# Kernel tuning notes

Measured on AMD Instinct MI355X. Metric: run time of the kernel, lower is better.

## Reference

```python
import jax, jax.numpy as jnp
import numpy as np

NUM_ITERATIONS = 3


def squash(t, axis=-1):
    # scale * t / sqrt(||t||^2 + eps), scale = ||t||^2 / (1 + ||t||^2)
    sq = jnp.sum(t * t, axis=axis, keepdims=True)
    return (sq / (1.0 + sq)) * t / jnp.sqrt(sq + 1e-8)


def setup_inputs() -> dict:
    key = jax.random.key(0)
    k1, k2 = jax.random.split(key)
    B, C, R, I, O = 128, 10, 8192, 8, 16
    x = jax.random.normal(k1, (B, R, I), dtype=jnp.float32)
    route_weights = jax.random.normal(k2, (C, R, I, O), dtype=jnp.float32) * 0.1
    return {"x": x, "route_weights": route_weights}


def reference(x, route_weights):
    # x: [B, R, I]; route_weights: [C, R, I, O]
    u_hat = jnp.einsum('bri,crio->bcro', x, route_weights)  # [B, C, R, O]
    B, C, R, O = u_hat.shape
    b_ij = jnp.zeros((B, C, R), dtype=u_hat.dtype)
    v_j = None
    for it in range(NUM_ITERATIONS):
        c_ij = jax.nn.softmax(b_ij, axis=1)                 # [B, C, R]
        s_j = jnp.einsum('bcr,bcro->bco', c_ij, u_hat)      # [B, C, O]
        v_j = squash(s_j, axis=-1)                          # [B, C, O]
        if it < NUM_ITERATIONS - 1:
            a_ij = jnp.einsum('bcro,bco->bcr', u_hat, v_j)  # [B, C, R]
            b_ij = b_ij + a_ij
    return v_j
```

## Files before the change

kernel.cpp:

```cpp
#include <hip/hip_runtime.h>
#include <hip/hip_fp16.h>
#include <math.h>

#define B_ 128
#define C_ 10
#define R_ 8192
#define I_ 8
#define O_ 16

typedef __attribute__((ext_vector_type(8))) _Float16 half8;
typedef __attribute__((ext_vector_type(16))) float f32x16;

#define XROW 512
#define WROW 64
#define WZERO 80
#define SBO (C_ * B_ * O_)

__device__ __forceinline__ unsigned pk2(float a, float b) {
    __half2 h = __floats2half2_rn(a, b);
    return *(unsigned*)&h;
}

__global__ __launch_bounds__(256, 4) void fused_iter(const float* __restrict__ x,
                                                     const float* __restrict__ w,
                                                     const float* __restrict__ vsum,
                                                     __half* __restrict__ part,
                                                     int mode) {
    __shared__ unsigned xls[8 * XROW];
    __shared__ unsigned wls[(80 + 1) * WROW];

    const int tid = threadIdx.x;
    const int wave = tid >> 6;
    const int lane = tid & 63;
    const int n = lane & 31;
    const int g = lane >> 5;
    const int rp_m = (lane & 31) >> 4;
    const int o_m = lane & 15;
    const int b = wave * 32 + n;
    const int r0 = blockIdx.x * 8;

#pragma unroll
    for (int k = 0; k < 8; ++k) {
        const int f = k * 256 + tid;
        const int bb = f >> 4;
        const int rr = (f >> 1) & 7;
        const int q = f & 1;
        const float4 v = *(const float4*)(x + ((size_t)bb * R_ + r0 + rr) * 8 + q * 4);
        *(uint2*)(xls + rr * XROW + bb * 4 + q * 2) = make_uint2(pk2(v.x, v.y), pk2(v.z, v.w));
    }
#pragma unroll
    for (int k = 0; k < 5; ++k) {
        const int id = k * 256 + tid;
        const int o = id & 15;
        const int r = (id >> 4) & 7;
        const int c = id >> 7;
        const float* wp = w + ((size_t)(c * R_ + r0 + r) * 8) * 16 + o;
        const float f0 = wp[0],  f1 = wp[16],  f2 = wp[32],  f3 = wp[48];
        const float f4 = wp[64], f5 = wp[80],  f6 = wp[96],  f7 = wp[112];
        *(uint4*)(wls + (c * 8 + r) * WROW + o * 4) =
            make_uint4(pk2(f0, f1), pk2(f2, f3), pk2(f4, f5), pk2(f6, f7));
    }
    if (tid < WROW) wls[WZERO * WROW + tid] = 0u;
    __syncthreads();

    const int act = (g == rp_m);

    half8 xbr[4];
#pragma unroll
    for (int rp = 0; rp < 4; ++rp)
        xbr[rp] = *(const half8*)(xls + (2 * rp + g) * XROW + b * 4);

    f32x16 zero16;
#pragma unroll
    for (int j = 0; j < 16; ++j) zero16[j] = 0.f;

    if (mode) {
        float dinv[4];
        {
            float dacc[4] = {0.f, 0.f, 0.f, 0.f};
#pragma unroll 1
            for (int c = 0; c < C_; ++c) {
                const float4* vp = (const float4*)(vsum + ((size_t)c * B_ + b) * O_ + 4 * g);
                const float4 va = vp[0];
                const float4 vb = vp[2];
#pragma unroll
                for (int rp = 0; rp < 4; ++rp) {
                    const int woff = act ? ((c * 8 + 2 * rp + g) * WROW + o_m * 4)
                                         : (WZERO * WROW);
                    const half8 a = *(const half8*)(wls + woff);
                    const f32x16 u = __builtin_amdgcn_mfma_f32_32x32x16_f16(a, xbr[rp], zero16, 0, 0, 0);
                    const float p0 = u[0] * va.x + u[1] * va.y + u[2] * va.z + u[3] * va.w
                                   + u[4] * vb.x + u[5] * vb.y + u[6] * vb.z + u[7] * vb.w;
                    const float p1 = u[8] * va.x + u[9] * va.y + u[10] * va.z + u[11] * va.w
                                   + u[12] * vb.x + u[13] * vb.y + u[14] * vb.z + u[15] * vb.w;
                    const float send = g ? p0 : p1;
                    const float recv = __shfl_xor(send, 32);
                    const float pg = (g ? p1 : p0) + recv;
                    dacc[rp] += __expf(pg);
                }
            }
#pragma unroll
            for (int rp = 0; rp < 4; ++rp) dinv[rp] = 1.0f / dacc[rp];
        }

#pragma unroll 1
        for (int c = 0; c < C_; ++c) {
            const float4* vp = (const float4*)(vsum + ((size_t)c * B_ + b) * O_ + 4 * g);
            const float4 va = vp[0];
            const float4 vb = vp[2];
            f32x16 acc;
#pragma unroll
            for (int rp = 0; rp < 4; ++rp) {
                const int woff = act ? ((c * 8 + 2 * rp + g) * WROW + o_m * 4)
                                     : (WZERO * WROW);
                const half8 a = *(const half8*)(wls + woff);
                const f32x16 u = __builtin_amdgcn_mfma_f32_32x32x16_f16(a, xbr[rp], zero16, 0, 0, 0);
                const float p0 = u[0] * va.x + u[1] * va.y + u[2] * va.z + u[3] * va.w
                               + u[4] * vb.x + u[5] * vb.y + u[6] * vb.z + u[7] * vb.w;
                const float p1 = u[8] * va.x + u[9] * va.y + u[10] * va.z + u[11] * va.w
                               + u[12] * vb.x + u[13] * vb.y + u[14] * vb.z + u[15] * vb.w;
                const float send = g ? p0 : p1;
                const float recv = __shfl_xor(send, 32);
                const float pg = (g ? p1 : p0) + recv;
                const float w_own = __expf(pg) * dinv[rp];
                const float w_oth = __shfl_xor(w_own, 32);
                const float c0 = g ? w_oth : w_own;
                const float c1 = g ? w_own : w_oth;
                if (rp == 0) {
#pragma unroll
                    for (int j = 0; j < 8; ++j)  acc[j] = c0 * u[j];
#pragma unroll
                    for (int j = 8; j < 16; ++j) acc[j] = c1 * u[j];
                } else {
#pragma unroll
                    for (int j = 0; j < 8; ++j)  acc[j] += c0 * u[j];
#pragma unroll
                    for (int j = 8; j < 16; ++j) acc[j] += c1 * u[j];
                }
            }
            const float f0 = acc[0] + acc[8],  f1 = acc[1] + acc[9];
            const float f2 = acc[2] + acc[10], f3 = acc[3] + acc[11];
            const float f4 = acc[4] + acc[12], f5 = acc[5] + acc[13];
            const float f6 = acc[6] + acc[14], f7 = acc[7] + acc[15];
            __half* pp = part + (((size_t)blockIdx.x * C_ + c) * B_ + b) * O_;
            *(uint2*)(pp + 4 * g)     = make_uint2(pk2(f0, f1), pk2(f2, f3));
            *(uint2*)(pp + 8 + 4 * g) = make_uint2(pk2(f4, f5), pk2(f6, f7));
        }
    } else {
#pragma unroll 1
        for (int c = 0; c < C_; ++c) {
            f32x16 acc = zero16;
#pragma unroll
            for (int rp = 0; rp < 4; ++rp) {
                const int woff = act ? ((c * 8 + 2 * rp + g) * WROW + o_m * 4)
                                     : (WZERO * WROW);
                const half8 a = *(const half8*)(wls + woff);
                acc = __builtin_amdgcn_mfma_f32_32x32x16_f16(a, xbr[rp], acc, 0, 0, 0);
            }
            const float f0 = (acc[0] + acc[8])  * 0.1f, f1 = (acc[1] + acc[9])  * 0.1f;
            const float f2 = (acc[2] + acc[10]) * 0.1f, f3 = (acc[3] + acc[11]) * 0.1f;
            const float f4 = (acc[4] + acc[12]) * 0.1f, f5 = (acc[5] + acc[13]) * 0.1f;
            const float f6 = (acc[6] + acc[14]) * 0.1f, f7 = (acc[7] + acc[15]) * 0.1f;
            __half* pp = part + (((size_t)blockIdx.x * C_ + c) * B_ + b) * O_;
            *(uint2*)(pp + 4 * g)     = make_uint2(pk2(f0, f1), pk2(f2, f3));
            *(uint2*)(pp + 8 + 4 * g) = make_uint2(pk2(f4, f5), pk2(f6, f7));
        }
    }
}

__global__ __launch_bounds__(256) void reduce1(const __half* __restrict__ part,
                                               float* __restrict__ part2) {
    const int t8 = blockIdx.x * 256 + threadIdx.x;
    const __half* p = part + (size_t)(blockIdx.y * 64) * SBO + (size_t)t8 * 8;
    float s0 = 0.f, s1 = 0.f, s2 = 0.f, s3 = 0.f;
    float s4 = 0.f, s5 = 0.f, s6 = 0.f, s7 = 0.f;
#pragma unroll 8
    for (int s = 0; s < 64; ++s) {
        const uint4 v = *(const uint4*)(p + (size_t)s * SBO);
        const __half2 h0 = *(const __half2*)&v.x;
        const __half2 h1 = *(const __half2*)&v.y;
        const __half2 h2 = *(const __half2*)&v.z;
        const __half2 h3 = *(const __half2*)&v.w;
        const float2 f0 = __half22float2(h0);
        const float2 f1 = __half22float2(h1);
        const float2 f2 = __half22float2(h2);
        const float2 f3 = __half22float2(h3);
        s0 += f0.x; s1 += f0.y; s2 += f1.x; s3 += f1.y;
        s4 += f2.x; s5 += f2.y; s6 += f3.x; s7 += f3.y;
    }
    float* q = part2 + (size_t)blockIdx.y * SBO + (size_t)t8 * 8;
    *(float4*)q       = make_float4(s0, s1, s2, s3);
    *(float4*)(q + 4) = make_float4(s4, s5, s6, s7);
}

__global__ __launch_bounds__(256) void finish_pass(const float* __restrict__ part2,
                                                   float* __restrict__ vsum,
                                                   float* __restrict__ out,
                                                   int mode) {
    const int t = blockIdx.x * 256 + threadIdx.x;
    float sum = 0.f;
#pragma unroll
    for (int s = 0; s < 16; ++s)
        sum += part2[(size_t)s * SBO + t];

    float sq = sum * sum;
    sq += __shfl_xor(sq, 1);
    sq += __shfl_xor(sq, 2);
    sq += __shfl_xor(sq, 4);
    sq += __shfl_xor(sq, 8);
    const float scale = sq / ((1.0f + sq) * sqrtf(sq + 1e-8f));
    const float v = scale * sum;

    if (mode == 0) {
        vsum[t] = v;
    } else if (mode == 1) {
        vsum[t] += v;
    } else {
        const int o = t & 15, b = (t >> 4) & 127, c = t >> 11;
        out[((size_t)b * C_ + c) * O_ + o] = v;
    }
}

extern "C" void kernel_launch(void* const* d_in, const int* in_sizes, int n_in,
                              void* d_out, int out_size, void* d_ws, size_t ws_size,
                              hipStream_t stream) {
    const float* x = (const float*)d_in[0];
    const float* w = (const float*)d_in[1];
    float* out = (float*)d_out;

    __half* part = (__half*)d_ws;
    float* part2 = (float*)(part + (size_t)1024 * SBO);
    float* vsum  = part2 + (size_t)16 * SBO;

    const dim3 fgrid(R_ / 8);
    const dim3 rgrid(10, 16);
    const dim3 ggrid(80);

    fused_iter<<<fgrid, 256, 0, stream>>>(x, w, vsum, part, 0);
    reduce1<<<rgrid, 256, 0, stream>>>(part, part2);
    finish_pass<<<ggrid, 256, 0, stream>>>(part2, vsum, out, 0);

    fused_iter<<<fgrid, 256, 0, stream>>>(x, w, vsum, part, 1);
    reduce1<<<rgrid, 256, 0, stream>>>(part, part2);
    finish_pass<<<ggrid, 256, 0, stream>>>(part2, vsum, out, 1);

    fused_iter<<<fgrid, 256, 0, stream>>>(x, w, vsum, part, 1);
    reduce1<<<rgrid, 256, 0, stream>>>(part, part2);
    finish_pass<<<ggrid, 256, 0, stream>>>(part2, vsum, out, 2);
}
```

Measured before the change: 218.6 us.

## Process two capsule classes per iteration, swizzle x LDS layout, widen reduction grid

The per-class loops now handle two classes per iteration, issuing two independent MFMAs so their latencies can overlap, and the weighted accumulation is folded directly into 8 accumulators. The x tile in LDS gets an XOR swizzle on the column index to reduce bank conflicts when each wave reads its B operand. The first-stage reduction uses 32 slices instead of 64 per block, giving twice as many blocks for better parallelism, while the finish pass now sums 32 partials instead of 16. Register pressure rises from holding two MFMA results at once, which may hurt occupancy under the 4-blocks launch bound.

Result: slower. 350.3 us (+60.3%).

```diff
diff --git a/kernel.cpp b/kernel.cpp
--- a/kernel.cpp
+++ b/kernel.cpp
@@ -15,10 +15,20 @@
 #define WROW 64
 #define WZERO 80
 #define SBO (C_ * B_ * O_)
+#define NRED 32
 
 __device__ __forceinline__ unsigned pk2(float a, float b) {
     __half2 h = __floats2half2_rn(a, b);
     return *(unsigned*)&h;
+}
+
+__device__ __forceinline__ float dot8lo(const f32x16& u, const float4& va, const float4& vb) {
+    return u[0] * va.x + u[1] * va.y + u[2] * va.z + u[3] * va.w
+         + u[4] * vb.x + u[5] * vb.y + u[6] * vb.z + u[7] * vb.w;
+}
+__device__ __forceinline__ float dot8hi(const f32x16& u, const float4& va, const float4& vb) {
+    return u[8] * va.x + u[9] * va.y + u[10] * va.z + u[11] * va.w
+         + u[12] * vb.x + u[13] * vb.y + u[14] * vb.z + u[15] * vb.w;
 }
 
 __global__ __launch_bounds__(256, 4) void fused_iter(const float* __restrict__ x,
@@ -46,7 +56,8 @@
         const int rr = (f >> 1) & 7;
         const int q = f & 1;
         const float4 v = *(const float4*)(x + ((size_t)bb * R_ + r0 + rr) * 8 + q * 4);
-        *(uint2*)(xls + rr * XROW + bb * 4 + q * 2) = make_uint2(pk2(v.x, v.y), pk2(v.z, v.w));
+        *(uint2*)(xls + rr * XROW + (((bb * 4 + q * 2) ^ (rr << 2)))) =
+            make_uint2(pk2(v.x, v.y), pk2(v.z, v.w));
     }
 #pragma unroll
     for (int k = 0; k < 5; ++k) {
@@ -67,8 +78,10 @@
 
     half8 xbr[4];
 #pragma unroll
-    for (int rp = 0; rp < 4; ++rp)
-        xbr[rp] = *(const half8*)(xls + (2 * rp + g) * XROW + b * 4);
+    for (int rp = 0; rp < 4; ++rp) {
+        const int row = 2 * rp + g;
+        xbr[rp] = *(const half8*)(xls + row * XROW + ((b * 4) ^ (row << 2)));
+    }
 
     f32x16 zero16;
 #pragma unroll
@@ -79,24 +92,28 @@
         {
             float dacc[4] = {0.f, 0.f, 0.f, 0.f};
 #pragma unroll 1
-            for (int c = 0; c < C_; ++c) {
-                const float4* vp = (const float4*)(vsum + ((size_t)c * B_ + b) * O_ + 4 * g);
-                const float4 va = vp[0];
-                const float4 vb = vp[2];
+            for (int c = 0; c < C_; c += 2) {
+                const float4* vpA = (const float4*)(vsum + ((size_t)c * B_ + b) * O_ + 4 * g);
+                const float4* vpB = (const float4*)(vsum + ((size_t)(c + 1) * B_ + b) * O_ + 4 * g);
+                const float4 vaA = vpA[0], vbA = vpA[2];
+                const float4 vaB = vpB[0], vbB = vpB[2];
 #pragma unroll
                 for (int rp = 0; rp < 4; ++rp) {
-                    const int woff = act ? ((c * 8 + 2 * rp + g) * WROW + o_m * 4)
-                                         : (WZERO * WROW);
-                    const half8 a = *(const half8*)(wls + woff);
-                    const f32x16 u = __builtin_amdgcn_mfma_f32_32x32x16_f16(a, xbr[rp], zero16, 0, 0, 0);
-                    const float p0 = u[0] * va.x + u[1] * va.y + u[2] * va.z + u[3] * va.w
-                                   + u[4] * vb.x + u[5] * vb.y + u[6] * vb.z + u[7] * vb.w;
-                    const float p1 = u[8] * va.x + u[9] * va.y + u[10] * va.z + u[11] * va.w
-                                   + u[12] * vb.x + u[13] * vb.y + u[14] * vb.z + u[15] * vb.w;
-                    const float send = g ? p0 : p1;
-                    const float recv = __shfl_xor(send, 32);
-                    const float pg = (g ? p1 : p0) + recv;
-                    dacc[rp] += __expf(pg);
+                    const int woffA = act ? ((c * 8 + 2 * rp + g) * WROW + o_m * 4)
+                                          : (WZERO * WROW);
+                    const int woffB = act ? (((c + 1) * 8 + 2 * rp + g) * WROW + o_m * 4)
+                                          : (WZERO * WROW);
+                    const half8 aA = *(const half8*)(wls + woffA);
+                    const half8 aB = *(const half8*)(wls + woffB);
+                    const f32x16 uA = __builtin_amdgcn_mfma_f32_32x32x16_f16(aA, xbr[rp], zero16, 0, 0, 0);
+                    const f32x16 uB = __builtin_amdgcn_mfma_f32_32x32x16_f16(aB, xbr[rp], zero16, 0, 0, 0);
+                    const float pA0 = dot8lo(uA, vaA, vbA), pA1 = dot8hi(uA, vaA, vbA);
+                    const float pB0 = dot8lo(uB, vaB, vbB), pB1 = dot8hi(uB, vaB, vbB);
+                    const float recvA = __shfl_xor(g ? pA0 : pA1, 32);
+                    const float recvB = __shfl_xor(g ? pB0 : pB1, 32);
+                    const float pgA = (g ? pA1 : pA0) + recvA;
+                    const float pgB = (g ? pB1 : pB0) + recvB;
+                    dacc[rp] += __expf(pgA) + __expf(pgB);
                 }
             }
 #pragma unroll
@@ -104,66 +121,74 @@
         }
 
 #pragma unroll 1
-        for (int c = 0; c < C_; ++c) {
-            const float4* vp = (const float4*)(vsum + ((size_t)c * B_ + b) * O_ + 4 * g);
-            const float4 va = vp[0];
-            const float4 vb = vp[2];
-            f32x16 acc;
+        for (int c = 0; c < C_; c += 2) {
+            const float4* vpA = (const float4*)(vsum + ((size_t)c * B_ + b) * O_ + 4 * g);
+            const float4* vpB = (const float4*)(vsum + ((size_t)(c + 1) * B_ + b) * O_ + 4 * g);
+            const float4 vaA = vpA[0], vbA = vpA[2];
+            const float4 vaB = vpB[0], vbB = vpB[2];
+            float accA[8], accB[8];
+#pragma unroll
+            for (int j = 0; j < 8; ++j) { accA[j] = 0.f; accB[j] = 0.f; }
 #pragma unroll
             for (int rp = 0; rp < 4; ++rp) {
-                const int woff = act ? ((c * 8 + 2 * rp + g) * WROW + o_m * 4)
-                                     : (WZERO * WROW);
-                const half8 a = *(const half8*)(wls + woff);
-                const f32x16 u = __builtin_amdgcn_mfma_f32_32x32x16_f16(a, xbr[rp], zero16, 0, 0, 0);
-                const float p0 = u[0] * va.x + u[1] * va.y + u[2] * va.z + u[3] * va.w
-                               + u[4] * vb.x + u[5] * vb.y + u[6] * vb.z + u[7] * vb.w;
-                const float p1 = u[8] * va.x + u[9] * va.y + u[10] * va.z + u[11] * va.w
-                               + u[12] * vb.x + u[13] * vb.y + u[14] * vb.z + u[15] * vb.w;
-                const float send = g ? p0 : p1;
-                const float recv = __shfl_xor(send, 32);
-                const float pg = (g ? p1 : p0) + recv;
-                const float w_own = __expf(pg) * dinv[rp];
-                const float w_oth = __shfl_xor(w_own, 32);
-                const float c0 = g ? w_oth : w_own;
-                const float c1 = g ? w_own : w_oth;
-                if (rp == 0) {
-#pragma unroll
-                    for (int j = 0; j < 8; ++j)  acc[j] = c0 * u[j];
-#pragma unroll
-                    for (int j = 8; j < 16; ++j) acc[j] = c1 * u[j];
-                } else {
-#pragma unroll
-                    for (int j = 0; j < 8; ++j)  acc[j] += c0 * u[j];
-#pragma unroll
-                    for (int j = 8; j < 16; ++j) acc[j] += c1 * u[j];
+                const int woffA = act ? ((c * 8 + 2 * rp + g) * WROW + o_m * 4)
+                                      : (WZERO * WROW);
+                const int woffB = act ? (((c + 1) * 8 + 2 * rp + g) * WROW + o_m * 4)
+                                      : (WZERO * WROW);
+                const half8 aA = *(const half8*)(wls + woffA);
+                const half8 aB = *(const half8*)(wls + woffB);
+                const f32x16 uA = __builtin_amdgcn_mfma_f32_32x32x16_f16(aA, xbr[rp], zero16, 0, 0, 0);
+                const f32x16 uB = __builtin_amdgcn_mfma_f32_32x32x16_f16(aB, xbr[rp], zero16, 0, 0, 0);
+                const float pA0 = dot8lo(uA, vaA, vbA), pA1 = dot8hi(uA, vaA, vbA);
+                const float pB0 = dot8lo(uB, vaB, vbB), pB1 = dot8hi(uB, vaB, vbB);
+                const float recvA = __shfl_xor(g ? pA0 : pA1, 32);
+                const float recvB = __shfl_xor(g ? pB0 : pB1, 32);
+                const float pgA = (g ? pA1 : pA0) + recvA;
+                const float pgB = (g ? pB1 : pB0) + recvB;
+                const float wA = __expf(pgA) * dinv[rp];
+                const float wB = __expf(pgB) * dinv[rp];
+                const float wAo = __shfl_xor(wA, 32);
+                const float wBo = __shfl_xor(wB, 32);
+                const float cA0 = g ? wAo : wA, cA1 = g ? wA : wAo;
+                const float cB0 = g ? wBo : wB, cB1 = g ? wB : wBo;
+#pragma unroll
+                for (int j = 0; j < 8; ++j) {
+                    accA[j] += cA0 * uA[j] + cA1 * uA[j + 8];
+                    accB[j] += cB0 * uB[j] + cB1 * uB[j + 8];
                 }
             }
-            const float f0 = acc[0] + acc[8],  f1 = acc[1] + acc[9];
-            const float f2 = acc[2] + acc[10], f3 = acc[3] + acc[11];
-            const float f4 = acc[4] + acc[12], f5 = acc[5] + acc[13];
-            const float f6 = acc[6] + acc[14], f7 = acc[7] + acc[15];
-            __half* pp = part + (((size_t)blockIdx.x * C_ + c) * B_ + b) * O_;
-            *(uint2*)(pp + 4 * g)     = make_uint2(pk2(f0, f1), pk2(f2, f3));
-            *(uint2*)(pp + 8 + 4 * g) = make_uint2(pk2(f4, f5), pk2(f6, f7));
+            __half* ppA = part + (((size_t)blockIdx.x * C_ + c) * B_ + b) * O_;
+            *(uint2*)(ppA + 4 * g)     = make_uint2(pk2(accA[0], accA[1]), pk2(accA[2], accA[3]));
+            *(uint2*)(ppA + 8 + 4 * g) = make_uint2(pk2(accA[4], accA[5]), pk2(accA[6], accA[7]));
+            __half* ppB = part + (((size_t)blockIdx.x * C_ + (c + 1)) * B_ + b) * O_;
+            *(uint2*)(ppB + 4 * g)     = make_uint2(pk2(accB[0], accB[1]), pk2(accB[2], accB[3]));
+            *(uint2*)(ppB + 8 + 4 * g) = make_uint2(pk2(accB[4], accB[5]), pk2(accB[6], accB[7]));
         }
     } else {
 #pragma unroll 1
-        for (int c = 0; c < C_; ++c) {
-            f32x16 acc = zero16;
+        for (int c = 0; c < C_; c += 2) {
+            f32x16 accA = zero16, accB = zero16;
 #pragma unroll
             for (int rp = 0; rp < 4; ++rp) {
-                const int woff = act ? ((c * 8 + 2 * rp + g) * WROW + o_m * 4)
-                                     : (WZERO * WROW);
-                const half8 a = *(const half8*)(wls + woff);
-                acc = __builtin_amdgcn_mfma_f32_32x32x16_f16(a, xbr[rp], acc, 0, 0, 0);
+                const int woffA = act ? ((c * 8 + 2 * rp + g) * WROW + o_m * 4)
+                                      : (WZERO * WROW);
+                const int woffB = act ? (((c + 1) * 8 + 2 * rp + g) * WROW + o_m * 4)
+                                      : (WZERO * WROW);
+                const half8 aA = *(const half8*)(wls + woffA);
+                const half8 aB = *(const half8*)(wls + woffB);
+                accA = __builtin_amdgcn_mfma_f32_32x32x16_f16(aA, xbr[rp], accA, 0, 0, 0);
+                accB = __builtin_amdgcn_mfma_f32_32x32x16_f16(aB, xbr[rp], accB, 0, 0, 0);
             }
-            const float f0 = (acc[0] + acc[8])  * 0.1f, f1 = (acc[1] + acc[9])  * 0.1f;
-            const float f2 = (acc[2] + acc[10]) * 0.1f, f3 = (acc[3] + acc[11]) * 0.1f;
-            const float f4 = (acc[4] + acc[12]) * 0.1f, f5 = (acc[5] + acc[13]) * 0.1f;
-            const float f6 = (acc[6] + acc[14]) * 0.1f, f7 = (acc[7] + acc[15]) * 0.1f;
-            __half* pp = part + (((size_t)blockIdx.x * C_ + c) * B_ + b) * O_;
-            *(uint2*)(pp + 4 * g)     = make_uint2(pk2(f0, f1), pk2(f2, f3));
-            *(uint2*)(pp + 8 + 4 * g) = make_uint2(pk2(f4, f5), pk2(f6, f7));
+            __half* ppA = part + (((size_t)blockIdx.x * C_ + c) * B_ + b) * O_;
+            *(uint2*)(ppA + 4 * g)     = make_uint2(pk2((accA[0] + accA[8]) * 0.1f, (accA[1] + accA[9]) * 0.1f),
+                                                    pk2((accA[2] + accA[10]) * 0.1f, (accA[3] + accA[11]) * 0.1f));
+            *(uint2*)(ppA + 8 + 4 * g) = make_uint2(pk2((accA[4] + accA[12]) * 0.1f, (accA[5] + accA[13]) * 0.1f),
+                                                    pk2((accA[6] + accA[14]) * 0.1f, (accA[7] + accA[15]) * 0.1f));
+            __half* ppB = part + (((size_t)blockIdx.x * C_ + (c + 1)) * B_ + b) * O_;
+            *(uint2*)(ppB + 4 * g)     = make_uint2(pk2((accB[0] + accB[8]) * 0.1f, (accB[1] + accB[9]) * 0.1f),
+                                                    pk2((accB[2] + accB[10]) * 0.1f, (accB[3] + accB[11]) * 0.1f));
+            *(uint2*)(ppB + 8 + 4 * g) = make_uint2(pk2((accB[4] + accB[12]) * 0.1f, (accB[5] + accB[13]) * 0.1f),
+                                                    pk2((accB[6] + accB[14]) * 0.1f, (accB[7] + accB[15]) * 0.1f));
         }
     }
 }
@@ -171,20 +196,16 @@
 __global__ __launch_bounds__(256) void reduce1(const __half* __restrict__ part,
                                                float* __restrict__ part2) {
     const int t8 = blockIdx.x * 256 + threadIdx.x;
-    const __half* p = part + (size_t)(blockIdx.y * 64) * SBO + (size_t)t8 * 8;
+    const __half* p = part + (size_t)(blockIdx.y * NRED) * SBO + (size_t)t8 * 8;
     float s0 = 0.f, s1 = 0.f, s2 = 0.f, s3 = 0.f;
     float s4 = 0.f, s5 = 0.f, s6 = 0.f, s7 = 0.f;
 #pragma unroll 8
-    for (int s = 0; s < 64; ++s) {
+    for (int s = 0; s < NRED; ++s) {
         const uint4 v = *(const uint4*)(p + (size_t)s * SBO);
-        const __half2 h0 = *(const __half2*)&v.x;
-        const __half2 h1 = *(const __half2*)&v.y;
-        const __half2 h2 = *(const __half2*)&v.z;
-        const __half2 h3 = *(const __half2*)&v.w;
-        const float2 f0 = __half22float2(h0);
-        const float2 f1 = __half22float2(h1);
-        const float2 f2 = __half22float2(h2);
-        const float2 f3 = __half22float2(h3);
+        const float2 f0 = __half22float2(*(const __half2*)&v.x);
+        const float2 f1 = __half22float2(*(const __half2*)&v.y);
+        const float2 f2 = __half22float2(*(const __half2*)&v.z);
+        const float2 f3 = __half22float2(*(const __half2*)&v.w);
         s0 += f0.x; s1 += f0.y; s2 += f1.x; s3 += f1.y;
         s4 += f2.x; s5 += f2.y; s6 += f3.x; s7 += f3.y;
     }
@@ -200,7 +221,7 @@
     const int t = blockIdx.x * 256 + threadIdx.x;
     float sum = 0.f;
 #pragma unroll
-    for (int s = 0; s < 16; ++s)
+    for (int s = 0; s < 1024 / NRED; ++s)
         sum += part2[(size_t)s * SBO + t];
 
     float sq = sum * sum;
@@ -230,10 +251,10 @@
 
     __half* part = (__half*)d_ws;
     float* part2 = (float*)(part + (size_t)1024 * SBO);
-    float* vsum  = part2 + (size_t)16 * SBO;
+    float* vsum  = part2 + (size_t)32 * SBO;
 
     const dim3 fgrid(R_ / 8);
-    const dim3 rgrid(10, 16);
+    const dim3 rgrid(10, 1024 / NRED);
     const dim3 ggrid(80);
 
     fused_iter<<<fgrid, 256, 0, stream>>>(x, w, vsum, part, 0);
```
